# Kernel tuning notes

Hardware: AMD Instinct MI355X
Metric: run time of the kernel (lower is better)

## Reference

```python
import jax, jax.numpy as jnp
import numpy as np
from jax import lax

DN = ('NCDHW', 'OIDHW', 'NCDHW')
BN_EPS = 1e-5  # eval-mode BatchNorm3d with running_mean=0, running_var=1


def conv3d(x, w, b):
    y = lax.conv_general_dilated(x, w, window_strides=(1, 1, 1),
                                 padding=[(1, 1)] * 3, dimension_numbers=DN)
    return y + b[None, :, None, None, None]


def maxpool2(x):
    return lax.reduce_window(x, -jnp.inf, lax.max,
                             (1, 1, 2, 2, 2), (1, 1, 2, 2, 2), 'VALID')


def spline_block(x, cw, cb, knots, sw, w1, w2, g, beta):
    # SplineConv3d: conv -> (BSpline3D blend with SiLU) -> BN(eval) -> maxpool
    y = conv3d(x, cw, cb)                                   # [b,c,d,h,w]
    basis = jnp.maximum(y[..., None] - knots, 0.0) ** 3     # [b,c,d,h,w,k]
    sp = jnp.einsum('bcdhwk,ck->bcdhw', basis, sw)
    out = (w1[None, :, None, None, None] * sp
           + w2[None, :, None, None, None] * (y * jax.nn.sigmoid(y)))
    scale = (g / jnp.sqrt(1.0 + BN_EPS))[None, :, None, None, None]
    return maxpool2(out * scale + beta[None, :, None, None, None])


def setup_inputs() -> dict:
    key = jax.random.key(0)
    ks = iter(jax.random.split(key, 40))
    def nrm(shape, s=1.0):
        return jax.random.normal(next(ks), shape, dtype=jnp.float32) * s
    d = {}
    d['x'] = nrm((2, 1, 64, 64, 64))
    for cin, cout, t in [(1, 32, '1'), (32, 64, '2'), (64, 128, '3')]:
        d[f'c{t}_w'] = nrm((cout, cin, 3, 3, 3), 0.1)
        d[f'c{t}_b'] = nrm((cout,), 0.01)
        d[f'c{t}_knots'] = jnp.linspace(-1.0, 1.0, 10).astype(jnp.float32)
        d[f'c{t}_sw'] = nrm((cout, 10), 0.2)
        d[f'c{t}_w1'] = nrm((cout,), 0.2)
        d[f'c{t}_w2'] = nrm((cout,), 0.2)
        d[f'bn{t}_g'] = 1.0 + nrm((cout,), 0.1)
        d[f'bn{t}_b'] = nrm((cout,), 0.1)
    d['fc1_w'] = nrm((256, 128), 0.05)
    d['fc1_b'] = nrm((256,), 0.01)
    d['fc2_w'] = nrm((2, 256), 0.05)
    d['fc2_b'] = nrm((2,), 0.01)
    return d


def reference(x,
              c1_w, c1_b, c1_knots, c1_sw, c1_w1, c1_w2, bn1_g, bn1_b,
              c2_w, c2_b, c2_knots, c2_sw, c2_w1, c2_w2, bn2_g, bn2_b,
              c3_w, c3_b, c3_knots, c3_sw, c3_w1, c3_w2, bn3_g, bn3_b,
              fc1_w, fc1_b, fc2_w, fc2_b):
    h = spline_block(x, c1_w, c1_b, c1_knots, c1_sw, c1_w1, c1_w2, bn1_g, bn1_b)
    h = spline_block(h, c2_w, c2_b, c2_knots, c2_sw, c2_w1, c2_w2, bn2_g, bn2_b)
    h = spline_block(h, c3_w, c3_b, c3_knots, c3_sw, c3_w1, c3_w2, bn3_g, bn3_b)
    h = h.mean(axis=(2, 3, 4))          # AdaptiveAvgPool3d((1,1,1)) + flatten
    h = jax.nn.relu(h @ fc1_w.T + fc1_b)  # dropout is identity in eval mode
    return h @ fc2_w.T + fc2_b
```

## Files before the change

### kernel.cpp

```cpp
#include <hip/hip_runtime.h>
#include <math.h>


#define GLOBAL_AS __attribute__((address_space(1)))
#define LDS_AS    __attribute__((address_space(3)))

static __device__ __forceinline__ void async_ld16(const float* g, float* l) {
    __builtin_amdgcn_global_load_lds((const GLOBAL_AS void*)g, (LDS_AS void*)l,
                                     16, 0, 0);
}

template <int TPB_, int CIN, int CSPLIT, int G, int PDT, int PHT, int PWT>
__global__ __launch_bounds__(TPB_, 2) void spline_block_kernel(
    const float* __restrict__ x,
    const float* __restrict__ cw,
    const float* __restrict__ cb,
    const float* __restrict__ knots,
    const float* __restrict__ sw,
    const float* __restrict__ w1,
    const float* __restrict__ w2,
    const float* __restrict__ g,
    const float* __restrict__ beta,
    const float* __restrict__ zbuf,
    float* __restrict__ out,
    int N, int Cout, int D, int H, int W,
    int ntiles, int nthw, int ntw)
{
    constexpr int SP     = PDT * PHT * PWT;
    constexpr int CPG    = CIN / CSPLIT;
    constexpr int ID     = 2 * PDT + 2;
    constexpr int IH     = 2 * PHT + 2;
    constexpr int PITCH  = 24;
    constexpr int ROWS   = ID * IH;
    constexpr int CHUNKS = ROWS * 6;
    constexpr int PHYS   = ROWS * PITCH;
    constexpr int NCH    = (CHUNKS + SP - 1) / SP;
    constexpr int BUFS   = (CPG > 1) ? 2 : 1;
    static_assert(SP * CSPLIT == TPB_, "block = CSPLIT x SP");
    static_assert(CIN % CSPLIT == 0, "cin divisible");
    static_assert(NCH <= 32, "mask fits u32");
    static_assert(CSPLIT == 1 ||
                  (CSPLIT - 1) * SP * G * 8 <= CSPLIT * BUFS * PHYS,
                  "reduction scratch fits in tile");

    __shared__ __align__(16) float tile[CSPLIT][BUFS][PHYS];
    __shared__ float  wlds[CIN * G * 28];
    __shared__ float4 stbl[G * 11];

    const int PD = D >> 1, PH = H >> 1, PW = W >> 1;
    const int groups = Cout / G;
    const int tid  = threadIdx.x;
    const int cg   = tid / SP;
    const int stid = tid % SP;

    const int bx      = blockIdx.x;
    const int tile_id = bx % ntiles;
    const int t1      = bx / ntiles;
    const int grp     = t1 % groups;
    const int n       = t1 / groups;
    const int c0      = grp * G;
    const int cinbase = cg * CPG;

    const int td  = tile_id / nthw;
    const int rem = tile_id % nthw;
    const int th_ = rem / ntw;
    const int tw_ = rem % ntw;

    for (int i = tid; i < CIN * G * 27; i += TPB_) {
        const int t  = i % 27;
        const int cgr = i / 27;
        const int gg = cgr % G;
        const int ci = cgr / G;
        wlds[cgr * 28 + t] = cw[((c0 + gg) * CIN + ci) * 27 + t];
    }
    for (int i = tid; i < G * 11; i += TPB_) {
        const int gg  = i / 11;
        const int cnt = i % 11;
        const int c   = c0 + gg;
        float A = 0.f, B3 = 0.f, C3 = 0.f, Dd = 0.f;
        for (int j = 0; j < cnt; j++) {
            const float s = sw[c * 10 + j];
            const float k = knots[j];
            A  += s;
            B3 += 3.0f * s * k;
            C3 += 3.0f * s * k * k;
            Dd += s * k * k * k;
        }
        stbl[i] = make_float4(A, B3, C3, Dd);
    }

    const int pwl = stid % PWT;
    const int phl = (stid / PWT) % PHT;
    const int pdl = stid / (PWT * PHT);

    const int pd0 = td * PDT, ph0 = th_ * PHT, pw0 = tw_ * PWT;
    const int d0 = 2 * pd0 - 1, h0 = 2 * ph0 - 1;
    const int w0 = 2 * pw0 - 1;
    const int wb = w0 & ~3;
    const int woff = w0 - wb;

    int off[NCH];
    unsigned vm = 0;
#pragma unroll
    for (int k = 0; k < NCH; k++) {
        const int chunk = stid + SP * k;
        const int row = chunk / 6, cs = chunk - row * 6;
        const int dz = row / IH, hy = row - dz * IH;
        const int dd = d0 + dz, hh = h0 + hy;
        const int wsd = wb + cs * 4;
        const bool ok = (chunk < CHUNKS) &
                        ((unsigned)dd < (unsigned)D) &
                        ((unsigned)hh < (unsigned)H) &
                        ((unsigned)wsd < (unsigned)W);
        off[k] = ok ? (dd * H + hh) * W + wsd : 0;
        vm |= (unsigned)ok << k;
    }

    const size_t chstride = (size_t)D * H * W;
    const float* xn = x + (size_t)n * CIN * chstride;

    float acc[G][8];
#pragma unroll
    for (int gg = 0; gg < G; gg++)
#pragma unroll
        for (int i = 0; i < 8; i++) acc[gg][i] = 0.0f;

    __syncthreads();

    {
        const float* xc = xn + (size_t)cinbase * chstride;
        float* dst = &tile[cg][0][0];
#pragma unroll
        for (int k = 0; k < NCH; k++) {
            const int chunk = stid + SP * k;
            if ((k + 1) * SP <= CHUNKS || chunk < CHUNKS) {
                const float* src = ((vm >> k) & 1) ? (xc + off[k]) : zbuf;
                async_ld16(src, dst + chunk * 4);
            }
        }
    }
    __syncthreads();

    int cur = 0;
#pragma unroll 1
    for (int s = 0; s < CPG; s++) {
        if (s + 1 < CPG) {
            const float* xc = xn + (size_t)(cinbase + s + 1) * chstride;
            float* dst = &tile[cg][cur ^ (BUFS - 1)][0];
#pragma unroll
            for (int k = 0; k < NCH; k++) {
                const int chunk = stid + SP * k;
                if ((k + 1) * SP <= CHUNKS || chunk < CHUNKS) {
                    const float* src = ((vm >> k) & 1) ? (xc + off[k]) : zbuf;
                    async_ld16(src, dst + chunk * 4);
                }
            }
        }

        const int ci = cinbase + s;
        const float* tb = &tile[cg][cur][0];
        float r[64];
#pragma unroll
        for (int dz = 0; dz < 4; dz++)
#pragma unroll
        for (int dy = 0; dy < 4; dy++) {
            const int rb = ((2 * pdl + dz) * IH + (2 * phl + dy)) * PITCH +
                           woff + 2 * pwl;
            r[(dz * 4 + dy) * 4 + 0] = tb[rb + 0];
            r[(dz * 4 + dy) * 4 + 1] = tb[rb + 1];
            r[(dz * 4 + dy) * 4 + 2] = tb[rb + 2];
            r[(dz * 4 + dy) * 4 + 3] = tb[rb + 3];
        }

#pragma unroll
        for (int gg = 0; gg < G; gg++) {
            const float4* w4p = (const float4*)&wlds[(ci * G + gg) * 28];
#pragma unroll
            for (int ch = 0; ch < 7; ch++) {
                const float4 wv = w4p[ch];
#pragma unroll
                for (int j = 0; j < 4; j++) {
                    const int tap = ch * 4 + j;
                    if (tap < 27) {
                        const float wvj = (j == 0) ? wv.x : (j == 1) ? wv.y
                                        : (j == 2) ? wv.z : wv.w;
                        const int kd = tap / 9, kh = (tap % 9) / 3, kw = tap % 3;
#pragma unroll
                        for (int od = 0; od < 2; od++)
#pragma unroll
                        for (int oh = 0; oh < 2; oh++)
#pragma unroll
                        for (int ow = 0; ow < 2; ow++)
                            acc[gg][(od * 2 + oh) * 2 + ow] =
                                fmaf(wvj,
                                     r[((od + kd) * 4 + (oh + kh)) * 4 + (ow + kw)],
                                     acc[gg][(od * 2 + oh) * 2 + ow]);
                    }
                }
            }
        }

        if (s + 1 < CPG) {
            __syncthreads();
            cur ^= 1;
        }
    }

    float* af = &acc[0][0];
    if (CSPLIT > 1) {
        __syncthreads();
        float* scratch = &tile[0][0][0];
        if (cg > 0) {
#pragma unroll
            for (int idx = 0; idx < G * 8; idx++)
                scratch[(idx * (CSPLIT - 1) + (cg - 1)) * SP + stid] = af[idx];
        }
        __syncthreads();
        if (cg == 0) {
#pragma unroll
            for (int idx = 0; idx < G * 8; idx++) {
                float s = af[idx];
                for (int j = 0; j < CSPLIT - 1; j++)
                    s += scratch[(idx * (CSPLIT - 1) + j) * SP + stid];
                af[idx] = s;
            }
        }
    }

    if (cg == 0) {
        const int pdg = pd0 + pdl, phg = ph0 + phl, pwg = pw0 + pwl;
#pragma unroll
        for (int gg = 0; gg < G; gg++) {
            const int c = c0 + gg;
            const float bias = cb[c];
            const float W1 = w1[c], W2 = w2[c];
            const float scale = g[c] * rsqrtf(1.0f + 1e-5f);
            const float bb = beta[c];

            float m = -INFINITY;
#pragma unroll
            for (int i = 0; i < 8; i++) {
                const float y = acc[gg][i] + bias;
                int idx = (int)floorf((y + 1.0f) * 4.5f) + 1;
                idx = min(max(idx, 0), 10);
                const float4 cf = stbl[gg * 11 + idx];
                const float sp = ((cf.x * y - cf.y) * y + cf.z) * y - cf.w;
                const float silu = y / (1.0f + __expf(-y));
                const float o = fmaf(W1 * sp + W2 * silu, scale, bb);
                m = fmaxf(m, o);
            }
            out[((size_t)(n * Cout + c) * PD + pdg) * PH * PW + phg * PW + pwg] = m;
        }
    }
}

__global__ __launch_bounds__(64) void mean_kernel(
    const float* __restrict__ h, float* __restrict__ out, int S)
{
    const int nc = blockIdx.x;
    const int lane = threadIdx.x;
    const float* p = h + (size_t)nc * S;
    float s = 0.0f;
    for (int i = lane; i < S; i += 64) s += p[i];
#pragma unroll
    for (int off = 32; off > 0; off >>= 1) s += __shfl_down(s, off, 64);
    if (lane == 0) out[nc] = s / (float)S;
}

__global__ __launch_bounds__(256) void fc_kernel(
    const float* __restrict__ pooled,
    const float* __restrict__ w1, const float* __restrict__ b1,
    const float* __restrict__ w2, const float* __restrict__ b2,
    float* __restrict__ out)
{
    __shared__ float hbuf[2][256];
    const int j = threadIdx.x;
#pragma unroll
    for (int nn = 0; nn < 2; nn++) {
        float s = b1[j];
        for (int k = 0; k < 128; k++)
            s = fmaf(pooled[nn * 128 + k], w1[j * 128 + k], s);
        hbuf[nn][j] = fmaxf(s, 0.0f);
    }
    __syncthreads();
    const int wid = j >> 6, lane = j & 63;
    const int nn = wid >> 1, oo = wid & 1;
    float s = 0.0f;
    for (int k = lane; k < 256; k += 64) s += hbuf[nn][k] * w2[oo * 256 + k];
#pragma unroll
    for (int off = 32; off > 0; off >>= 1) s += __shfl_down(s, off, 64);
    if (lane == 0) out[nn * 2 + oo] = s + b2[oo];
}

extern "C" void kernel_launch(void* const* d_in, const int* in_sizes, int n_in,
                              void* d_out, int out_size, void* d_ws, size_t ws_size,
                              hipStream_t stream) {
    const float* x      = (const float*)d_in[0];
    const float* c1_w   = (const float*)d_in[1];
    const float* c1_b   = (const float*)d_in[2];
    const float* c1_kn  = (const float*)d_in[3];
    const float* c1_sw  = (const float*)d_in[4];
    const float* c1_w1  = (const float*)d_in[5];
    const float* c1_w2  = (const float*)d_in[6];
    const float* bn1_g  = (const float*)d_in[7];
    const float* bn1_b  = (const float*)d_in[8];
    const float* c2_w   = (const float*)d_in[9];
    const float* c2_b   = (const float*)d_in[10];
    const float* c2_kn  = (const float*)d_in[11];
    const float* c2_sw  = (const float*)d_in[12];
    const float* c2_w1  = (const float*)d_in[13];
    const float* c2_w2  = (const float*)d_in[14];
    const float* bn2_g  = (const float*)d_in[15];
    const float* bn2_b  = (const float*)d_in[16];
    const float* c3_w   = (const float*)d_in[17];
    const float* c3_b   = (const float*)d_in[18];
    const float* c3_kn  = (const float*)d_in[19];
    const float* c3_sw  = (const float*)d_in[20];
    const float* c3_w1  = (const float*)d_in[21];
    const float* c3_w2  = (const float*)d_in[22];
    const float* bn3_g  = (const float*)d_in[23];
    const float* bn3_b  = (const float*)d_in[24];
    const float* fc1_w  = (const float*)d_in[25];
    const float* fc1_b  = (const float*)d_in[26];
    const float* fc2_w  = (const float*)d_in[27];
    const float* fc2_b  = (const float*)d_in[28];

    float* ws = (float*)d_ws;
    float* h1     = ws;
    float* h2     = h1 + 2097152;
    float* h3     = h2 + 524288;
    float* pooled = h3 + 131072;
    float* zbuf   = pooled + 256;

    hipMemsetAsync(zbuf, 0, 64, stream);

    spline_block_kernel<256, 1, 1, 4, 4, 8, 8><<<dim3(2048), dim3(256), 0, stream>>>(
        x, c1_w, c1_b, c1_kn, c1_sw, c1_w1, c1_w2, bn1_g, bn1_b, zbuf, h1,
        2, 32, 64, 64, 64, 128, 16, 4);
    spline_block_kernel<256, 32, 4, 4, 2, 4, 8><<<dim3(2048), dim3(256), 0, stream>>>(
        h1, c2_w, c2_b, c2_kn, c2_sw, c2_w1, c2_w2, bn2_g, bn2_b, zbuf, h2,
        2, 64, 32, 32, 32, 64, 8, 2);
    spline_block_kernel<256, 64, 4, 4, 2, 4, 8><<<dim3(512), dim3(256), 0, stream>>>(
        h2, c3_w, c3_b, c3_kn, c3_sw, c3_w1, c3_w2, bn3_g, bn3_b, zbuf, h3,
        2, 128, 16, 16, 16, 8, 2, 1);
    mean_kernel<<<dim3(256), dim3(64), 0, stream>>>(h3, pooled, 512);
    fc_kernel<<<dim3(1), dim3(256), 0, stream>>>(pooled, fc1_w, fc1_b, fc2_w, fc2_b,
                                                 (float*)d_out);
}
```

Baseline: 372.9 us.

## Store intermediate activations with padded rows so conv tiles load aligned

Layer outputs h1 and h2 now go into W-padded buffers (pitch 36 and 20) with a one-column zero halo. The next layer's tile loads then start at 16-byte aligned offsets with five chunks per row instead of six, need no W bounds checks, and read LDS as float2. Layer 2 also changes tiling to CSPLIT=1 with a larger spatial tile and fewer blocks. The cost is two extra memsets of the padded buffers each call and different occupancy and parallelism in layer 2.

```diff
diff --git a/kernel.cpp b/kernel.cpp
--- a/kernel.cpp
+++ b/kernel.cpp
@@ -10,7 +10,7 @@
                                      16, 0, 0);
 }
 
-template <int TPB_, int CIN, int CSPLIT, int G, int PDT, int PHT, int PWT>
+template <int TPB_, int CIN, int CSPLIT, int G, int PDT, int PHT, int PWT, bool AL>
 __global__ __launch_bounds__(TPB_, 2) void spline_block_kernel(
     const float* __restrict__ x,
     const float* __restrict__ cw,
@@ -23,22 +23,25 @@
     const float* __restrict__ beta,
     const float* __restrict__ zbuf,
     float* __restrict__ out,
-    int N, int Cout, int D, int H, int W,
+    int N, int Cout, int D, int H, int W, int WP,
+    int OWP, int OWO,
     int ntiles, int nthw, int ntw)
 {
     constexpr int SP     = PDT * PHT * PWT;
     constexpr int CPG    = CIN / CSPLIT;
     constexpr int ID     = 2 * PDT + 2;
     constexpr int IH     = 2 * PHT + 2;
-    constexpr int PITCH  = 24;
+    constexpr int CPR    = AL ? 5 : 6;
+    constexpr int PITCH  = CPR * 4;
     constexpr int ROWS   = ID * IH;
-    constexpr int CHUNKS = ROWS * 6;
+    constexpr int CHUNKS = ROWS * CPR;
     constexpr int PHYS   = ROWS * PITCH;
     constexpr int NCH    = (CHUNKS + SP - 1) / SP;
     constexpr int BUFS   = (CPG > 1) ? 2 : 1;
     static_assert(SP * CSPLIT == TPB_, "block = CSPLIT x SP");
     static_assert(CIN % CSPLIT == 0, "cin divisible");
     static_assert(NCH <= 32, "mask fits u32");
+    static_assert(!AL || (PWT % 8) == 0, "aligned path needs 16-dword tile step");
     static_assert(CSPLIT == 1 ||
                   (CSPLIT - 1) * SP * G * 8 <= CSPLIT * BUFS * PHYS,
                   "reduction scratch fits in tile");
@@ -96,27 +99,27 @@
     const int pd0 = td * PDT, ph0 = th_ * PHT, pw0 = tw_ * PWT;
     const int d0 = 2 * pd0 - 1, h0 = 2 * ph0 - 1;
     const int w0 = 2 * pw0 - 1;
-    const int wb = w0 & ~3;
-    const int woff = w0 - wb;
+    const int sorg  = AL ? (2 * pw0) : (w0 & ~3);
+    const int woff  = AL ? 0 : (w0 - sorg);
 
     int off[NCH];
     unsigned vm = 0;
 #pragma unroll
     for (int k = 0; k < NCH; k++) {
         const int chunk = stid + SP * k;
-        const int row = chunk / 6, cs = chunk - row * 6;
+        const int row = chunk / CPR, cs = chunk - row * CPR;
         const int dz = row / IH, hy = row - dz * IH;
         const int dd = d0 + dz, hh = h0 + hy;
-        const int wsd = wb + cs * 4;
-        const bool ok = (chunk < CHUNKS) &
-                        ((unsigned)dd < (unsigned)D) &
-                        ((unsigned)hh < (unsigned)H) &
-                        ((unsigned)wsd < (unsigned)W);
-        off[k] = ok ? (dd * H + hh) * W + wsd : 0;
+        const int wsd = sorg + cs * 4;
+        bool ok = (chunk < CHUNKS) &
+                  ((unsigned)dd < (unsigned)D) &
+                  ((unsigned)hh < (unsigned)H);
+        if (!AL) ok = ok & ((unsigned)wsd < (unsigned)W);
+        off[k] = ok ? (dd * H + hh) * WP + wsd : 0;
         vm |= (unsigned)ok << k;
     }
 
-    const size_t chstride = (size_t)D * H * W;
+    const size_t chstride = (size_t)D * H * WP;
     const float* xn = x + (size_t)n * CIN * chstride;
 
     float acc[G][8];
@@ -166,10 +169,19 @@
         for (int dy = 0; dy < 4; dy++) {
             const int rb = ((2 * pdl + dz) * IH + (2 * phl + dy)) * PITCH +
                            woff + 2 * pwl;
-            r[(dz * 4 + dy) * 4 + 0] = tb[rb + 0];
-            r[(dz * 4 + dy) * 4 + 1] = tb[rb + 1];
-            r[(dz * 4 + dy) * 4 + 2] = tb[rb + 2];
-            r[(dz * 4 + dy) * 4 + 3] = tb[rb + 3];
+            if (AL) {
+                const float2 v0 = *(const float2*)(tb + rb);
+                const float2 v1 = *(const float2*)(tb + rb + 2);
+                r[(dz * 4 + dy) * 4 + 0] = v0.x;
+                r[(dz * 4 + dy) * 4 + 1] = v0.y;
+                r[(dz * 4 + dy) * 4 + 2] = v1.x;
+                r[(dz * 4 + dy) * 4 + 3] = v1.y;
+            } else {
+                r[(dz * 4 + dy) * 4 + 0] = tb[rb + 0];
+                r[(dz * 4 + dy) * 4 + 1] = tb[rb + 1];
+                r[(dz * 4 + dy) * 4 + 2] = tb[rb + 2];
+                r[(dz * 4 + dy) * 4 + 3] = tb[rb + 3];
+            }
         }
 
 #pragma unroll
@@ -249,7 +261,8 @@
                 const float o = fmaf(W1 * sp + W2 * silu, scale, bb);
                 m = fmaxf(m, o);
             }
-            out[((size_t)(n * Cout + c) * PD + pdg) * PH * PW + phg * PW + pwg] = m;
+            out[(((size_t)(n * Cout + c) * PD + pdg) * PH + phg) * OWP + OWO + pwg]
+                = m;
         }
     }
 }
@@ -327,22 +340,27 @@
 
     float* ws = (float*)d_ws;
     float* h1     = ws;
-    float* h2     = h1 + 2097152;
-    float* h3     = h2 + 524288;
+    float* h2     = h1 + 2359296;
+    float* h3     = h2 + 655360;
     float* pooled = h3 + 131072;
     float* zbuf   = pooled + 256;
 
     hipMemsetAsync(zbuf, 0, 64, stream);
-
-    spline_block_kernel<256, 1, 1, 4, 4, 8, 8><<<dim3(2048), dim3(256), 0, stream>>>(
+    hipMemsetAsync(h1, 0, 2359296 * sizeof(float), stream);
+    hipMemsetAsync(h2, 0, 655360 * sizeof(float), stream);
+
+    spline_block_kernel<256, 1, 1, 4, 4, 8, 8, false>
+        <<<dim3(2048), dim3(256), 0, stream>>>(
         x, c1_w, c1_b, c1_kn, c1_sw, c1_w1, c1_w2, bn1_g, bn1_b, zbuf, h1,
-        2, 32, 64, 64, 64, 128, 16, 4);
-    spline_block_kernel<256, 32, 4, 4, 2, 4, 8><<<dim3(2048), dim3(256), 0, stream>>>(
+        2, 32, 64, 64, 64, 64, 36, 1, 128, 16, 4);
+    spline_block_kernel<256, 32, 1, 4, 4, 8, 8, true>
+        <<<dim3(512), dim3(256), 0, stream>>>(
         h1, c2_w, c2_b, c2_kn, c2_sw, c2_w1, c2_w2, bn2_g, bn2_b, zbuf, h2,
-        2, 64, 32, 32, 32, 64, 8, 2);
-    spline_block_kernel<256, 64, 4, 4, 2, 4, 8><<<dim3(512), dim3(256), 0, stream>>>(
+        2, 64, 32, 32, 32, 36, 20, 1, 16, 4, 2);
+    spline_block_kernel<256, 64, 4, 4, 2, 4, 8, true>
+        <<<dim3(512), dim3(256), 0, stream>>>(
         h2, c3_w, c3_b, c3_kn, c3_sw, c3_w1, c3_w2, bn3_g, bn3_b, zbuf, h3,
-        2, 128, 16, 16, 16, 8, 2, 1);
+        2, 128, 16, 16, 16, 20, 8, 0, 8, 2, 1);
     mean_kernel<<<dim3(256), dim3(64), 0, stream>>>(h3, pooled, 512);
     fc_kernel<<<dim3(1), dim3(256), 0, stream>>>(pooled, fc1_w, fc1_b, fc2_w, fc2_b,
                                                  (float*)d_out);
```

New measurement: 342.6 us. -8.1%, faster.
